# Kernel tuning notes

Hardware: AMD Instinct MI355X
Metric: run time of the kernel (lower is better)

## Reference

```python
import jax, jax.numpy as jnp
import numpy as np

D_HEAD = 64

def setup_inputs() -> dict:
    key = jax.random.key(0)
    k1, k2, k3, k4, k5 = jax.random.split(key, 5)
    B, S, D, H, Dh = 2, 2048, 1024, 16, D_HEAD
    std = 0.02
    return {
        "residual": jax.random.normal(k1, (B, S, D), dtype=jnp.float32),
        "W_Q": jax.random.normal(k2, (H, Dh, D), dtype=jnp.float32) * std,
        "W_K": jax.random.normal(k3, (H, Dh, D), dtype=jnp.float32) * std,
        "W_V": jax.random.normal(k4, (H, Dh, D), dtype=jnp.float32) * std,
        "W_O": jax.random.normal(k5, (H, Dh, D), dtype=jnp.float32) * std,
    }

def reference(residual, W_Q, W_K, W_V, W_O):
    # residual: [b, s, d]; W_*: [h, e, d] with e = d_head
    S = residual.shape[1]
    q = jnp.einsum('bsd,hed->bshe', residual, W_Q)
    k = jnp.einsum('bsd,hed->bshe', residual, W_K)
    v = jnp.einsum('bsd,hed->bshe', residual, W_V)
    scale = 1.0 / jnp.sqrt(jnp.asarray(D_HEAD, dtype=residual.dtype))
    scores = jnp.einsum('bqhe,bkhe->bhqk', q, k) * scale  # [b,h,s,s]
    causal = jnp.tril(jnp.ones((S, S), dtype=bool))
    scores = jnp.where(causal, scores, -jnp.inf)
    pattern = jax.nn.softmax(scores, axis=-1)
    attn_out = jnp.einsum('bhqk,bkhe->bqhe', pattern, v)
    out = jnp.einsum('bqhe,hed->bqd', attn_out, W_O)
    return out
```

## Files before the change

### kernel.cpp

```cpp
#include <hip/hip_runtime.h>
#include <math.h>

typedef unsigned short bf16;
typedef __attribute__((ext_vector_type(8))) short short8;
typedef __attribute__((ext_vector_type(4))) float f32x4;

#define S_LEN 2048
#define NH    16
#define DH    64
#define DM    1024
#define BATCH 2

__device__ __forceinline__ bf16 f2bf(float f) {
    unsigned u = __float_as_uint(f);
    u += 0x7fffu + ((u >> 16) & 1u);
    return (bf16)(u >> 16);
}

__device__ __forceinline__ unsigned pack2(float a, float b) {
    unsigned ua = __float_as_uint(a) + 0x8000u;
    unsigned ub = __float_as_uint(b) + 0x8000u;
    return (ua >> 16) | (ub & 0xFFFF0000u);
}

__device__ __forceinline__ float fast_exp2(float x) {
#if __has_builtin(__builtin_amdgcn_exp2f)
    return __builtin_amdgcn_exp2f(x);
#else
    return exp2f(x);
#endif
}

__device__ __forceinline__ void gload_lds16(const void* g, void* s) {
    __builtin_amdgcn_global_load_lds(
        (const __attribute__((address_space(1))) unsigned int*)g,
        (__attribute__((address_space(3))) unsigned int*)s, 16, 0, 0);
}

#define QSCALE 0.18033688011112042f

__global__ __launch_bounds__(256) void convert_kernel(
    const float* __restrict__ X,  const float* __restrict__ WQ,
    const float* __restrict__ WK, const float* __restrict__ WV,
    const float* __restrict__ WO,
    bf16* __restrict__ Xb, bf16* __restrict__ WQb, bf16* __restrict__ WKb,
    bf16* __restrict__ WVb, bf16* __restrict__ WOt)
{
    __shared__ float T[64][65];
    const int blk = blockIdx.x;
    if (blk < 7168) {
        const int t = blk * 256 + threadIdx.x;
        if (t < 1048576) {
            float4 v = ((const float4*)X)[t];
            unsigned long long pk = (unsigned long long)f2bf(v.x)
                | ((unsigned long long)f2bf(v.y) << 16)
                | ((unsigned long long)f2bf(v.z) << 32)
                | ((unsigned long long)f2bf(v.w) << 48);
            *(unsigned long long*)(Xb + 4 * (size_t)t) = pk;
        } else if (t < 1310720) {
            int i = t - 1048576;
            float4 v = ((const float4*)WQ)[i];
            unsigned long long pk = (unsigned long long)f2bf(v.x * QSCALE)
                | ((unsigned long long)f2bf(v.y * QSCALE) << 16)
                | ((unsigned long long)f2bf(v.z * QSCALE) << 32)
                | ((unsigned long long)f2bf(v.w * QSCALE) << 48);
            *(unsigned long long*)(WQb + 4 * (size_t)i) = pk;
        } else if (t < 1572864) {
            int i = t - 1310720;
            float4 v = ((const float4*)WK)[i];
            unsigned long long pk = (unsigned long long)f2bf(v.x)
                | ((unsigned long long)f2bf(v.y) << 16)
                | ((unsigned long long)f2bf(v.z) << 32)
                | ((unsigned long long)f2bf(v.w) << 48);
            *(unsigned long long*)(WKb + 4 * (size_t)i) = pk;
        } else {
            int i = t - 1572864;
            float4 v = ((const float4*)WV)[i];
            unsigned long long pk = (unsigned long long)f2bf(v.x)
                | ((unsigned long long)f2bf(v.y) << 16)
                | ((unsigned long long)f2bf(v.z) << 32)
                | ((unsigned long long)f2bf(v.w) << 48);
            *(unsigned long long*)(WVb + 4 * (size_t)i) = pk;
        }
    } else {
        const int tile = blk - 7168;
        const int he0 = (tile & 15) * 64, d0 = (tile >> 4) * 64;
        const int tid = threadIdx.x;
        const int row = tid >> 2, c0 = (tid & 3) * 16;
        #pragma unroll
        for (int u = 0; u < 4; ++u) {
            float4 v = *(const float4*)(WO + (size_t)(he0 + row) * DM + d0 + c0 + u * 4);
            T[row][c0 + u * 4 + 0] = v.x;
            T[row][c0 + u * 4 + 1] = v.y;
            T[row][c0 + u * 4 + 2] = v.z;
            T[row][c0 + u * 4 + 3] = v.w;
        }
        __syncthreads();
        bf16 tmp[16];
        #pragma unroll
        for (int j = 0; j < 16; ++j) tmp[j] = f2bf(T[c0 + j][row]);
        *(short8*)(WOt + (size_t)(d0 + row) * DM + he0 + c0)     = *(short8*)&tmp[0];
        *(short8*)(WOt + (size_t)(d0 + row) * DM + he0 + c0 + 8) = *(short8*)&tmp[8];
    }
}

__global__ __launch_bounds__(256) void proj_kernel(
    const bf16* __restrict__ Xb, const bf16* __restrict__ WQb,
    const bf16* __restrict__ WKb, const bf16* __restrict__ WVb,
    bf16* __restrict__ qbuf, bf16* __restrict__ kbuf, bf16* __restrict__ vt)
{
    __shared__ char lds[32768];
    char* As = lds;
    char* Bs = lds + 16384;

    const int id = blockIdx.x;
    const int tid = threadIdx.x, wave = tid >> 6, lane = tid & 63;
    const int tx = lane & 15, quad = lane >> 4;
    const int wm = (wave >> 1) * 64, wn = (wave & 1) * 64;

    int mode, m0, n0, bb = 0;
    const bf16 *Aop, *Bop;
    if (id < 512) {
        mode = id & 1;
        int rem = id >> 1;
        m0 = (rem & 31) * 128;
        n0 = (rem >> 5) * 128;
        Aop = Xb + (size_t)m0 * DM;
        Bop = (mode ? WKb : WQb) + (size_t)n0 * DM;
    } else {
        mode = 2;
        int rem = id - 512;
        bb = rem & 1;
        rem >>= 1;
        m0 = (rem & 7) * 128;
        n0 = (rem >> 3) * 128;
        Aop = WVb + (size_t)m0 * DM;
        Bop = Xb + ((size_t)bb * S_LEN + n0) * DM;
    }

    f32x4 acc[4][4] = {};

    for (int k0 = 0; k0 < DM; k0 += 64) {
        #pragma unroll
        for (int r = 0; r < 4; ++r) {
            int slot = r * 256 + tid;
            int row = slot >> 3, g = slot & 7, gl = g ^ (row & 7);
            gload_lds16(Aop + (size_t)row * DM + k0 + gl * 8,
                        As + r * 4096 + wave * 1024);
            gload_lds16(Bop + (size_t)row * DM + k0 + gl * 8,
                        Bs + r * 4096 + wave * 1024);
        }
        __syncthreads();
        #pragma unroll
        for (int ks = 0; ks < 2; ++ks) {
            const int swz = ((ks * 4 + quad) ^ (tx & 7)) * 16;
            short8 af[4], bfr[4];
            #pragma unroll
            for (int mt = 0; mt < 4; ++mt)
                af[mt] = *(const short8*)(As + (wm + mt * 16 + tx) * 128 + swz);
            #pragma unroll
            for (int nt = 0; nt < 4; ++nt)
                bfr[nt] = *(const short8*)(Bs + (wn + nt * 16 + tx) * 128 + swz);
            #pragma unroll
            for (int mt = 0; mt < 4; ++mt)
                #pragma unroll
                for (int nt = 0; nt < 4; ++nt)
                    acc[mt][nt] = __builtin_amdgcn_mfma_f32_16x16x32_bf16(
                        af[mt], bfr[nt], acc[mt][nt], 0, 0, 0);
        }
        __syncthreads();
    }

    if (mode < 2) {
        bf16* outb = mode ? kbuf : qbuf;
        #pragma unroll
        for (int mt = 0; mt < 4; ++mt)
            #pragma unroll
            for (int nt = 0; nt < 4; ++nt)
                #pragma unroll
                for (int r = 0; r < 4; ++r) {
                    int mG = m0 + wm + mt * 16 + quad * 4 + r;
                    int nG = n0 + wn + nt * 16 + tx;
                    int b = mG >> 11, s = mG & 2047, h = nG >> 6, e = nG & 63;
                    outb[((size_t)(b * NH + h) * S_LEN + s) * DH + e] =
                        f2bf(acc[mt][nt][r]);
                }
    } else {
        #pragma unroll
        for (int mt = 0; mt < 4; ++mt)
            #pragma unroll
            for (int nt = 0; nt < 4; ++nt)
                #pragma unroll
                for (int r = 0; r < 4; ++r) {
                    int he = m0 + wm + mt * 16 + quad * 4 + r;
                    int s  = n0 + wn + nt * 16 + tx;
                    vt[((size_t)bb * DM + he) * S_LEN + s] = f2bf(acc[mt][nt][r]);
                }
    }
}

__global__ __launch_bounds__(256) void flash_kernel(
    const bf16* __restrict__ qbuf, const bf16* __restrict__ kbuf,
    const bf16* __restrict__ vtb, bf16* __restrict__ attn)
{
    __shared__ char lds[49152];
    char* Pts = lds + 32768;

    const int i  = blockIdx.x;
    const int bh = i & 31;
    const int j  = i >> 5;
    const int qb = (i < 256) ? (15 - j) : (j - 8);
    const int tid = threadIdx.x, wave = tid >> 6, lane = tid & 63;
    const int tx = lane & 15, quad = lane >> 4;
    const int sw = tx & 7;

    const bf16* Qg = qbuf + (size_t)bh * S_LEN * DH + (size_t)qb * 128 * DH;
    const bf16* Kg = kbuf + (size_t)bh * S_LEN * DH;
    const bf16* Vg = vtb  + (size_t)bh * DH * S_LEN;

    short8 bq[2][2];
    #pragma unroll
    for (int g = 0; g < 2; ++g)
        #pragma unroll
        for (int es = 0; es < 2; ++es)
            bq[g][es] = *(const short8*)(Qg + (size_t)(wave * 32 + g * 16 + tx) * DH +
                                         (es * 4 + quad) * 8);

    f32x4 oacc[2][4] = {};
    float l_part[2] = {0.0f, 0.0f};

    const int kmax  = 2 * qb + 1;
    const int wdiag = 2 * qb + (wave >> 1);
    const int qg0   = qb * 128 + wave * 32 + tx;

    char* Pw = Pts + wave * 4096;

    {
        char* Kb = lds;
        char* Vb = lds + 8192;
        #pragma unroll
        for (int r = 0; r < 2; ++r) {
            int slot = r * 256 + tid;
            int row = slot >> 3, g = slot & 7, gl = g ^ (row & 7);
            gload_lds16(Kg + (size_t)row * DH + gl * 8, Kb + r * 4096 + wave * 1024);
            gload_lds16(Vg + (size_t)row * S_LEN + gl * 8, Vb + r * 4096 + wave * 1024);
        }
    }

    for (int kt64 = 0; kt64 <= kmax; ++kt64) {
        char* Kc = lds + (kt64 & 1) * 16384;
        char* Vc = Kc + 8192;
        __syncthreads();

        if (kt64 < kmax) {
            char* Kn = lds + ((kt64 + 1) & 1) * 16384;
            char* Vn = Kn + 8192;
            #pragma unroll
            for (int r = 0; r < 2; ++r) {
                int slot = r * 256 + tid;
                int row = slot >> 3, g = slot & 7, gl = g ^ (row & 7);
                gload_lds16(Kg + ((size_t)(kt64 + 1) * 64 + row) * DH + gl * 8,
                            Kn + r * 4096 + wave * 1024);
                gload_lds16(Vg + (size_t)row * S_LEN + (kt64 + 1) * 64 + gl * 8,
                            Vn + r * 4096 + wave * 1024);
            }
        }

        if (kt64 <= wdiag) {
            f32x4 st[2][4] = {};
            #pragma unroll
            for (int es = 0; es < 2; ++es) {
                #pragma unroll
                for (int kt = 0; kt < 4; ++kt) {
                    short8 ak = *(const short8*)(Kc + (kt * 16 + tx) * 128 +
                                                 (((es * 4 + quad) ^ sw) * 16));
                    #pragma unroll
                    for (int g = 0; g < 2; ++g)
                        st[g][kt] = __builtin_amdgcn_mfma_f32_16x16x32_bf16(
                            ak, bq[g][es], st[g][kt], 0, 0, 0);
                }
            }

            if (kt64 == wdiag) {
                #pragma unroll
                for (int g = 0; g < 2; ++g)
                    #pragma unroll
                    for (int kt = 0; kt < 4; ++kt)
                        #pragma unroll
                        for (int r = 0; r < 4; ++r)
                            if (kt64 * 64 + kt * 16 + quad * 4 + r > qg0 + g * 16)
                                st[g][kt][r] = -1e30f;
            }

            #pragma unroll
            for (int g = 0; g < 2; ++g) {
                float rs = 0.0f;
                #pragma unroll
                for (int kt = 0; kt < 4; ++kt) {
                    #pragma unroll
                    for (int r = 0; r < 4; ++r) {
                        float p = fast_exp2(st[g][kt][r]);
                        st[g][kt][r] = p;
                        rs += p;
                    }
                    unsigned lo = pack2(st[g][kt][0], st[g][kt][1]);
                    unsigned hi = pack2(st[g][kt][2], st[g][kt][3]);
                    int kg = kt * 2 + (quad >> 1);
                    *(uint2*)(Pw + (g * 16 + tx) * 128 + ((kg ^ sw) * 16) +
                              (quad & 1) * 8) = make_uint2(lo, hi);
                }
                l_part[g] += rs;
            }
            asm volatile("s_waitcnt lgkmcnt(0)" ::: "memory");

            #pragma unroll
            for (int ks = 0; ks < 2; ++ks) {
                const int swz = ((ks * 4 + quad) ^ sw) * 16;
                short8 bp[2];
                #pragma unroll
                for (int g = 0; g < 2; ++g)
                    bp[g] = *(const short8*)(Pw + (g * 16 + tx) * 128 + swz);
                #pragma unroll
                for (int et = 0; et < 4; ++et) {
                    short8 av = *(const short8*)(Vc + (et * 16 + tx) * 128 + swz);
                    #pragma unroll
                    for (int g = 0; g < 2; ++g)
                        oacc[g][et] = __builtin_amdgcn_mfma_f32_16x16x32_bf16(
                            av, bp[g], oacc[g][et], 0, 0, 0);
                }
            }
        }
    }

    const int b = bh >> 4, h = bh & 15;
    #pragma unroll
    for (int g = 0; g < 2; ++g) {
        float l = l_part[g];
        l += __shfl_xor(l, 16);
        l += __shfl_xor(l, 32);
        float inv = 1.0f / l;
        #pragma unroll
        for (int et = 0; et < 4; ++et) {
            unsigned lo = pack2(oacc[g][et][0] * inv, oacc[g][et][1] * inv);
            unsigned hi = pack2(oacc[g][et][2] * inv, oacc[g][et][3] * inv);
            int eg = et * 2 + (quad >> 1);
            *(uint2*)(Pw + (g * 16 + tx) * 128 + ((eg ^ sw) * 16) +
                      (quad & 1) * 8) = make_uint2(lo, hi);
        }
    }
    asm volatile("s_waitcnt lgkmcnt(0)" ::: "memory");

    #pragma unroll
    for (int g = 0; g < 2; ++g) {
        const int s = qb * 128 + wave * 32 + g * 16 + tx;
        bf16* op = attn + ((size_t)b * S_LEN + s) * DM + h * DH;
        #pragma unroll
        for (int c2 = 0; c2 < 2; ++c2) {
            int c = quad + c2 * 4;
            short8 v = *(const short8*)(Pw + (g * 16 + tx) * 128 + ((c ^ sw) * 16));
            *(short8*)(op + c * 8) = v;
        }
    }
}

__global__ __launch_bounds__(256) void out_proj_kernel(
    const bf16* __restrict__ A, const bf16* __restrict__ Bt,
    float* __restrict__ out)
{
    __shared__ char lds[24576];
    char* As = lds;
    char* Bs = lds + 16384;

    const int m0 = blockIdx.x * 128, n0 = blockIdx.y * 64;
    const int tid = threadIdx.x, wave = tid >> 6, lane = tid & 63;
    const int tx = lane & 15, quad = lane >> 4;
    const int wm = wave * 32;

    f32x4 acc[2][4] = {};

    for (int k0 = 0; k0 < DM; k0 += 64) {
        #pragma unroll
        for (int r = 0; r < 4; ++r) {
            int slot = r * 256 + tid;
            int row = slot >> 3, g = slot & 7, gl = g ^ (row & 7);
            gload_lds16(A + (size_t)(m0 + row) * DM + k0 + gl * 8,
                        As + r * 4096 + wave * 1024);
        }
        #pragma unroll
        for (int r = 0; r < 2; ++r) {
            int slot = r * 256 + tid;
            int row = slot >> 3, g = slot & 7, gl = g ^ (row & 7);
            gload_lds16(Bt + (size_t)(n0 + row) * DM + k0 + gl * 8,
                        Bs + r * 4096 + wave * 1024);
        }
        __syncthreads();
        #pragma unroll
        for (int ks = 0; ks < 2; ++ks) {
            const int swz = ((ks * 4 + quad) ^ (tx & 7)) * 16;
            short8 af[2], bfr[4];
            #pragma unroll
            for (int mt = 0; mt < 2; ++mt)
                af[mt] = *(const short8*)(As + (wm + mt * 16 + tx) * 128 + swz);
            #pragma unroll
            for (int nt = 0; nt < 4; ++nt)
                bfr[nt] = *(const short8*)(Bs + (nt * 16 + tx) * 128 + swz);
            #pragma unroll
            for (int mt = 0; mt < 2; ++mt)
                #pragma unroll
                for (int nt = 0; nt < 4; ++nt)
                    acc[mt][nt] = __builtin_amdgcn_mfma_f32_16x16x32_bf16(
                        af[mt], bfr[nt], acc[mt][nt], 0, 0, 0);
        }
        __syncthreads();
    }

    #pragma unroll
    for (int mt = 0; mt < 2; ++mt)
        #pragma unroll
        for (int nt = 0; nt < 4; ++nt)
            #pragma unroll
            for (int r = 0; r < 4; ++r) {
                int mG = m0 + wm + mt * 16 + quad * 4 + r;
                int nG = n0 + nt * 16 + tx;
                out[(size_t)mG * DM + nG] = acc[mt][nt][r];
            }
}

extern "C" void kernel_launch(void* const* d_in, const int* in_sizes, int n_in,
                              void* d_out, int out_size, void* d_ws, size_t ws_size,
                              hipStream_t stream) {
    const float* X  = (const float*)d_in[0];
    const float* WQ = (const float*)d_in[1];
    const float* WK = (const float*)d_in[2];
    const float* WV = (const float*)d_in[3];
    const float* WO = (const float*)d_in[4];
    float* out = (float*)d_out;

    char* ws = (char*)d_ws;
    bf16* Xb   = (bf16*)(ws);
    bf16* WQb  = (bf16*)(ws + (8u  << 20));
    bf16* WKb  = (bf16*)(ws + (10u << 20));
    bf16* WVb  = (bf16*)(ws + (12u << 20));
    bf16* WOt  = (bf16*)(ws + (14u << 20));
    bf16* qbuf = (bf16*)(ws + (16u << 20));
    bf16* kbuf = (bf16*)(ws + (24u << 20));
    bf16* vt   = (bf16*)(ws + (32u << 20));
    bf16* attn = (bf16*)(ws + (40u << 20));

    convert_kernel<<<7424, 256, 0, stream>>>(X, WQ, WK, WV, WO,
                                             Xb, WQb, WKb, WVb, WOt);
    proj_kernel<<<768, 256, 0, stream>>>(Xb, WQb, WKb, WVb, qbuf, kbuf, vt);
    flash_kernel<<<512, 256, 0, stream>>>(qbuf, kbuf, vt, attn);
    out_proj_kernel<<<dim3(32, 16), 256, 0, stream>>>(attn, WOt, out);
}
```

Baseline: 177.0 us.

## Double-buffer LDS in projection GEMMs and vectorize QKV epilogue stores

Both the QKV projection and output projection GEMMs now use two LDS stages. The next K-tile's global-to-LDS loads are issued before the MFMA work on the current tile, and one barrier per iteration replaces two. The projection kernel also swaps its A and B operands, so each lane's four accumulator values are contiguous in the output layout and can be written as one packed 8-byte store instead of four scalar bf16 stores. This doubles LDS use per block, which may lower occupancy. Correctness relies on the single barrier ordering reads of the old buffer before it is overwritten.

Result: faster. 171.1 us (-3.3%).

```diff
diff --git a/kernel.cpp b/kernel.cpp
--- a/kernel.cpp
+++ b/kernel.cpp
@@ -2,6 +2,7 @@
 #include <math.h>
 
 typedef unsigned short bf16;
+typedef unsigned long long u64;
 typedef __attribute__((ext_vector_type(8))) short short8;
 typedef __attribute__((ext_vector_type(4))) float f32x4;
 
@@ -21,6 +22,10 @@
     unsigned ua = __float_as_uint(a) + 0x8000u;
     unsigned ub = __float_as_uint(b) + 0x8000u;
     return (ua >> 16) | (ub & 0xFFFF0000u);
+}
+
+__device__ __forceinline__ u64 pack4(f32x4 v) {
+    return (u64)pack2(v[0], v[1]) | ((u64)pack2(v[2], v[3]) << 32);
 }
 
 __device__ __forceinline__ float fast_exp2(float x) {
@@ -52,35 +57,27 @@
         const int t = blk * 256 + threadIdx.x;
         if (t < 1048576) {
             float4 v = ((const float4*)X)[t];
-            unsigned long long pk = (unsigned long long)f2bf(v.x)
-                | ((unsigned long long)f2bf(v.y) << 16)
-                | ((unsigned long long)f2bf(v.z) << 32)
-                | ((unsigned long long)f2bf(v.w) << 48);
-            *(unsigned long long*)(Xb + 4 * (size_t)t) = pk;
+            u64 pk = (u64)f2bf(v.x) | ((u64)f2bf(v.y) << 16)
+                   | ((u64)f2bf(v.z) << 32) | ((u64)f2bf(v.w) << 48);
+            *(u64*)(Xb + 4 * (size_t)t) = pk;
         } else if (t < 1310720) {
             int i = t - 1048576;
             float4 v = ((const float4*)WQ)[i];
-            unsigned long long pk = (unsigned long long)f2bf(v.x * QSCALE)
-                | ((unsigned long long)f2bf(v.y * QSCALE) << 16)
-                | ((unsigned long long)f2bf(v.z * QSCALE) << 32)
-                | ((unsigned long long)f2bf(v.w * QSCALE) << 48);
-            *(unsigned long long*)(WQb + 4 * (size_t)i) = pk;
+            u64 pk = (u64)f2bf(v.x * QSCALE) | ((u64)f2bf(v.y * QSCALE) << 16)
+                   | ((u64)f2bf(v.z * QSCALE) << 32) | ((u64)f2bf(v.w * QSCALE) << 48);
+            *(u64*)(WQb + 4 * (size_t)i) = pk;
         } else if (t < 1572864) {
             int i = t - 1310720;
             float4 v = ((const float4*)WK)[i];
-            unsigned long long pk = (unsigned long long)f2bf(v.x)
-                | ((unsigned long long)f2bf(v.y) << 16)
-                | ((unsigned long long)f2bf(v.z) << 32)
-                | ((unsigned long long)f2bf(v.w) << 48);
-            *(unsigned long long*)(WKb + 4 * (size_t)i) = pk;
+            u64 pk = (u64)f2bf(v.x) | ((u64)f2bf(v.y) << 16)
+                   | ((u64)f2bf(v.z) << 32) | ((u64)f2bf(v.w) << 48);
+            *(u64*)(WKb + 4 * (size_t)i) = pk;
         } else {
             int i = t - 1572864;
             float4 v = ((const float4*)WV)[i];
-            unsigned long long pk = (unsigned long long)f2bf(v.x)
-                | ((unsigned long long)f2bf(v.y) << 16)
-                | ((unsigned long long)f2bf(v.z) << 32)
-                | ((unsigned long long)f2bf(v.w) << 48);
-            *(unsigned long long*)(WVb + 4 * (size_t)i) = pk;
+            u64 pk = (u64)f2bf(v.x) | ((u64)f2bf(v.y) << 16)
+                   | ((u64)f2bf(v.z) << 32) | ((u64)f2bf(v.w) << 48);
+            *(u64*)(WVb + 4 * (size_t)i) = pk;
         }
     } else {
         const int tile = blk - 7168;
@@ -109,48 +106,67 @@
     const bf16* __restrict__ WKb, const bf16* __restrict__ WVb,
     bf16* __restrict__ qbuf, bf16* __restrict__ kbuf, bf16* __restrict__ vt)
 {
-    __shared__ char lds[32768];
-    char* As = lds;
-    char* Bs = lds + 16384;
+    __shared__ char lds[65536];
 
     const int id = blockIdx.x;
     const int tid = threadIdx.x, wave = tid >> 6, lane = tid & 63;
     const int tx = lane & 15, quad = lane >> 4;
     const int wm = (wave >> 1) * 64, wn = (wave & 1) * 64;
 
-    int mode, m0, n0, bb = 0;
+    int mode, am0, bn0, bb = 0;
     const bf16 *Aop, *Bop;
     if (id < 512) {
         mode = id & 1;
         int rem = id >> 1;
-        m0 = (rem & 31) * 128;
-        n0 = (rem >> 5) * 128;
-        Aop = Xb + (size_t)m0 * DM;
-        Bop = (mode ? WKb : WQb) + (size_t)n0 * DM;
+        bn0 = (rem & 31) * 128;
+        am0 = (rem >> 5) * 128;
+        Aop = (mode ? WKb : WQb) + (size_t)am0 * DM;
+        Bop = Xb + (size_t)bn0 * DM;
     } else {
         mode = 2;
         int rem = id - 512;
         bb = rem & 1;
         rem >>= 1;
-        m0 = (rem & 7) * 128;
-        n0 = (rem >> 3) * 128;
-        Aop = WVb + (size_t)m0 * DM;
-        Bop = Xb + ((size_t)bb * S_LEN + n0) * DM;
+        bn0 = (rem & 7) * 128;
+        am0 = (rem >> 3) * 128;
+        Aop = Xb + ((size_t)bb * S_LEN + am0) * DM;
+        Bop = WVb + (size_t)bn0 * DM;
     }
 
     f32x4 acc[4][4] = {};
 
-    for (int k0 = 0; k0 < DM; k0 += 64) {
+    {
+        char* As = lds;
+        char* Bs = lds + 16384;
         #pragma unroll
         for (int r = 0; r < 4; ++r) {
             int slot = r * 256 + tid;
             int row = slot >> 3, g = slot & 7, gl = g ^ (row & 7);
-            gload_lds16(Aop + (size_t)row * DM + k0 + gl * 8,
-                        As + r * 4096 + wave * 1024);
-            gload_lds16(Bop + (size_t)row * DM + k0 + gl * 8,
-                        Bs + r * 4096 + wave * 1024);
-        }
+            gload_lds16(Aop + (size_t)row * DM + gl * 8, As + r * 4096 + wave * 1024);
+            gload_lds16(Bop + (size_t)row * DM + gl * 8, Bs + r * 4096 + wave * 1024);
+        }
+    }
+
+    for (int kt = 0; kt < 16; ++kt) {
+        char* As = lds + (kt & 1) * 32768;
+        char* Bs = As + 16384;
         __syncthreads();
+
+        if (kt < 15) {
+            char* An = lds + ((kt + 1) & 1) * 32768;
+            char* Bn = An + 16384;
+            const int k0 = (kt + 1) * 64;
+            #pragma unroll
+            for (int r = 0; r < 4; ++r) {
+                int slot = r * 256 + tid;
+                int row = slot >> 3, g = slot & 7, gl = g ^ (row & 7);
+                gload_lds16(Aop + (size_t)row * DM + k0 + gl * 8,
+                            An + r * 4096 + wave * 1024);
+                gload_lds16(Bop + (size_t)row * DM + k0 + gl * 8,
+                            Bn + r * 4096 + wave * 1024);
+            }
+        }
+
         #pragma unroll
         for (int ks = 0; ks < 2; ++ks) {
             const int swz = ((ks * 4 + quad) ^ (tx & 7)) * 16;
@@ -168,7 +184,6 @@
                     acc[mt][nt] = __builtin_amdgcn_mfma_f32_16x16x32_bf16(
                         af[mt], bfr[nt], acc[mt][nt], 0, 0, 0);
         }
-        __syncthreads();
     }
 
     if (mode < 2) {
@@ -176,26 +191,24 @@
         #pragma unroll
         for (int mt = 0; mt < 4; ++mt)
             #pragma unroll
-            for (int nt = 0; nt < 4; ++nt)
-                #pragma unroll
-                for (int r = 0; r < 4; ++r) {
-                    int mG = m0 + wm + mt * 16 + quad * 4 + r;
-                    int nG = n0 + wn + nt * 16 + tx;
-                    int b = mG >> 11, s = mG & 2047, h = nG >> 6, e = nG & 63;
-                    outb[((size_t)(b * NH + h) * S_LEN + s) * DH + e] =
-                        f2bf(acc[mt][nt][r]);
-                }
+            for (int nt = 0; nt < 4; ++nt) {
+                int heG  = am0 + wm + mt * 16 + quad * 4;
+                int tokG = bn0 + wn + nt * 16 + tx;
+                int b = tokG >> 11, s = tokG & 2047;
+                int h = heG >> 6, e0 = heG & 63;
+                *(u64*)(outb + ((size_t)(b * NH + h) * S_LEN + s) * DH + e0) =
+                    pack4(acc[mt][nt]);
+            }
     } else {
         #pragma unroll
         for (int mt = 0; mt < 4; ++mt)
             #pragma unroll
-            for (int nt = 0; nt < 4; ++nt)
-                #pragma unroll
-                for (int r = 0; r < 4; ++r) {
-                    int he = m0 + wm + mt * 16 + quad * 4 + r;
-                    int s  = n0 + wn + nt * 16 + tx;
-                    vt[((size_t)bb * DM + he) * S_LEN + s] = f2bf(acc[mt][nt][r]);
-                }
+            for (int nt = 0; nt < 4; ++nt) {
+                int sG  = am0 + wm + mt * 16 + quad * 4;
+                int heG = bn0 + wn + nt * 16 + tx;
+                *(u64*)(vt + ((size_t)bb * DM + heG) * S_LEN + sG) =
+                    pack4(acc[mt][nt]);
+            }
     }
 }
 
@@ -367,9 +380,7 @@
     const bf16* __restrict__ A, const bf16* __restrict__ Bt,
     float* __restrict__ out)
 {
-    __shared__ char lds[24576];
-    char* As = lds;
-    char* Bs = lds + 16384;
+    __shared__ char lds[49152];
 
     const int m0 = blockIdx.x * 128, n0 = blockIdx.y * 64;
     const int tid = threadIdx.x, wave = tid >> 6, lane = tid & 63;
@@ -378,22 +389,50 @@
 
     f32x4 acc[2][4] = {};
 
-    for (int k0 = 0; k0 < DM; k0 += 64) {
+    {
+        char* As = lds;
+        char* Bs = lds + 16384;
         #pragma unroll
         for (int r = 0; r < 4; ++r) {
             int slot = r * 256 + tid;
             int row = slot >> 3, g = slot & 7, gl = g ^ (row & 7);
-            gload_lds16(A + (size_t)(m0 + row) * DM + k0 + gl * 8,
+            gload_lds16(A + (size_t)(m0 + row) * DM + gl * 8,
                         As + r * 4096 + wave * 1024);
         }
         #pragma unroll
         for (int r = 0; r < 2; ++r) {
             int slot = r * 256 + tid;
             int row = slot >> 3, g = slot & 7, gl = g ^ (row & 7);
-            gload_lds16(Bt + (size_t)(n0 + row) * DM + k0 + gl * 8,
+            gload_lds16(Bt + (size_t)(n0 + row) * DM + gl * 8,
                         Bs + r * 4096 + wave * 1024);
         }
+    }
+
+    for (int kt = 0; kt < 16; ++kt) {
+        char* As = lds + (kt & 1) * 24576;
+        char* Bs = As + 16384;
         __syncthreads();
+
+        if (kt < 15) {
+            char* An = lds + ((kt + 1) & 1) * 24576;
+            char* Bn = An + 16384;
+            const int k0 = (kt + 1) * 64;
+            #pragma unroll
+            for (int r = 0; r < 4; ++r) {
+                int slot = r * 256 + tid;
+                int row = slot >> 3, g = slot & 7, gl = g ^ (row & 7);
+                gload_lds16(A + (size_t)(m0 + row) * DM + k0 + gl * 8,
+                            An + r * 4096 + wave * 1024);
+            }
+            #pragma unroll
+            for (int r = 0; r < 2; ++r) {
+                int slot = r * 256 + tid;
+                int row = slot >> 3, g = slot & 7, gl = g ^ (row & 7);
+                gload_lds16(Bt + (size_t)(n0 + row) * DM + k0 + gl * 8,
+                            Bn + r * 4096 + wave * 1024);
+            }
+        }
+
         #pragma unroll
         for (int ks = 0; ks < 2; ++ks) {
             const int swz = ((ks * 4 + quad) ^ (tx & 7)) * 16;
@@ -411,7 +450,6 @@
                     acc[mt][nt] = __builtin_amdgcn_mfma_f32_16x16x32_bf16(
                         af[mt], bfr[nt], acc[mt][nt], 0, 0, 0);
         }
-        __syncthreads();
     }
 
     #pragma unroll
```
